# Optimization experiments

Measured on AMD Instinct MI355X. Metric: run time of the kernel, lower is better.

Reference implementation:

```python
import jax, jax.numpy as jnp
import numpy as np

B, S, K, D = 4096, 32, 1024, 128
DECAY, EPS = 0.99, 1e-05


def setup_inputs() -> dict:
    key = jax.random.key(0)
    k1, k2, k3 = jax.random.split(key, 3)
    indices = jax.random.randint(k1, (B, S), 0, K)
    embedding = jax.random.normal(k2, (S, K, D), dtype=jnp.float32)
    ema_cluster_size = jnp.zeros((S, K), dtype=jnp.float32)
    ema_w = jax.random.normal(k3, (S, K, D), dtype=jnp.float32)
    return {"indices": indices, "embedding": embedding,
            "ema_cluster_size": ema_cluster_size, "ema_w": ema_w}


def reference(indices, embedding, ema_cluster_size, ema_w):
    # embedding: [S, K, D]; indices: [B, S]
    s_idx = jnp.broadcast_to(jnp.arange(S), indices.shape)  # [B, S]

    # gather: z_q[b, s] = embedding[s, indices[b, s]]
    z_q = embedding[s_idx, indices]  # [B, S, D]

    # cluster_size = one_hot(indices, K).sum(0)  ==  histogram per state slot
    counts = jnp.zeros((S, K), embedding.dtype).at[s_idx, indices].add(1.0)

    # dw = einsum('bsk,bsd->skd', one_hot, z_q)  ==  scatter-add of z_q into codes
    dw = jnp.zeros((S, K, D), embedding.dtype).at[s_idx, indices].add(z_q)

    new_ecs = DECAY * ema_cluster_size + (1.0 - DECAY) * counts        # [S, K]
    new_ema_w = DECAY * ema_w + (1.0 - DECAY) * dw                     # [S, K, D]

    n = new_ecs.sum(axis=-1, keepdims=True)                            # [S, 1]
    cluster_size = (new_ecs + EPS) / (n + K * EPS) * n                 # Laplace-smoothed
    new_embedding = new_ema_w / cluster_size[..., None]                # [S, K, D]

    return z_q, new_embedding, new_ecs, new_ema_w
```

## Files before the change

### kernel.cpp

```cpp
#include <hip/hip_runtime.h>

#define B_ 4096
#define S_ 32
#define K_ 1024
#define D_ 128
constexpr float DECAY = 0.99f;
constexpr float OMD   = 0.01f;
constexpr float EPS   = 1e-5f;

typedef float f4 __attribute__((ext_vector_type(4)));
typedef int   i4 __attribute__((ext_vector_type(4)));


__global__ void __launch_bounds__(256)
init_kernel(const float* __restrict__ ecs_in,
            int* __restrict__ counts,
            float* __restrict__ n_out) {
    const int s = blockIdx.x;
    const int t = threadIdx.x;
    reinterpret_cast<i4*>(counts + s * K_)[t] = i4{0, 0, 0, 0};
    const f4 v = reinterpret_cast<const f4*>(ecs_in + s * K_)[t];
    float local = v.x + v.y + v.z + v.w;
#pragma unroll
    for (int off = 1; off < 64; off <<= 1) local += __shfl_xor(local, off);
    __shared__ float red[4];
    if ((t & 63) == 0) red[t >> 6] = local;
    __syncthreads();
    if (t == 0)
        n_out[s] = DECAY * (red[0] + red[1] + red[2] + red[3]) + OMD * (float)B_;
}

__global__ void __launch_bounds__(256)
gather_hist_kernel(const int* __restrict__ idx,
                   const float* __restrict__ emb,
                   float* __restrict__ z_q,
                   int* __restrict__ counts) {
    const int s     = blockIdx.x & (S_ - 1);
    const int chunk = blockIdx.x >> 5;
    const int g     = threadIdx.x >> 5;
    const int lane  = threadIdx.x & 31;
    const int b     = chunk * 8 + g;
    const int row   = b * S_ + s;
    const int k     = idx[row];
    if (lane == 0) atomicAdd(&counts[s * K_ + k], 1);
    const f4 val =
        reinterpret_cast<const f4*>(emb)[((size_t)s * K_ + k) * 32 + lane];
    __builtin_nontemporal_store(
        val, reinterpret_cast<f4*>(z_q) + (size_t)row * 32 + lane);
}

__global__ void __launch_bounds__(256)
ema_kernel(const float* __restrict__ ema_w,
           const float* __restrict__ emb,
           const float* __restrict__ ecs_in,
           const int* __restrict__ counts,
           const float* __restrict__ n_arr,
           float* __restrict__ new_ecs_out,
           float* __restrict__ new_ema_w_out,
           float* __restrict__ new_emb_out) {
    const int i = blockIdx.x;
    const int s = i & (S_ - 1);
    const int c = i >> 5;
    const size_t base = ((size_t)s * K_ + c * 32) * 32;
    const float n = n_arr[s];
    const float denom_inv = 1.0f / (n + (float)K_ * EPS);
#pragma unroll
    for (int it = 0; it < 4; ++it) {
        const size_t e = base + it * 256 + threadIdx.x;
        const int sk = (int)(e >> 5);
        const float ccount = (float)counts[sk];
        const float ne = DECAY * ecs_in[sk] + OMD * ccount;
        const float cs = (ne + EPS) * denom_inv * n;
        if ((e & 31) == 0) new_ecs_out[sk] = ne;

        const f4 w  = reinterpret_cast<const f4*>(ema_w)[e];
        const f4 em = reinterpret_cast<const f4*>(emb)[e];
        f4 nw;
        nw.x = DECAY * w.x + OMD * ccount * em.x;
        nw.y = DECAY * w.y + OMD * ccount * em.y;
        nw.z = DECAY * w.z + OMD * ccount * em.z;
        nw.w = DECAY * w.w + OMD * ccount * em.w;
        __builtin_nontemporal_store(
            nw, reinterpret_cast<f4*>(new_ema_w_out) + e);
        const float inv = 1.0f / cs;
        f4 nb;
        nb.x = nw.x * inv;
        nb.y = nw.y * inv;
        nb.z = nw.z * inv;
        nb.w = nw.w * inv;
        __builtin_nontemporal_store(
            nb, reinterpret_cast<f4*>(new_emb_out) + e);
    }
}

extern "C" void kernel_launch(void* const* d_in, const int* in_sizes, int n_in,
                              void* d_out, int out_size, void* d_ws, size_t ws_size,
                              hipStream_t stream) {
    const int*   idx   = (const int*)d_in[0];
    const float* emb   = (const float*)d_in[1];
    const float* ecs   = (const float*)d_in[2];
    const float* ema_w = (const float*)d_in[3];

    float* out       = (float*)d_out;
    float* z_q       = out;
    float* new_emb   = z_q + (size_t)B_ * S_ * D_;
    float* new_ecs   = new_emb + (size_t)S_ * K_ * D_;
    float* new_ema_w = new_ecs + (size_t)S_ * K_;

    int*   counts = (int*)d_ws;
    float* n_arr  = (float*)d_ws + (size_t)S_ * K_;

    init_kernel<<<S_, 256, 0, stream>>>(ecs, counts, n_arr);
    gather_hist_kernel<<<(B_ * S_) / 8, 256, 0, stream>>>(idx, emb, z_q, counts);
    ema_kernel<<<1024, 256, 0, stream>>>(
        ema_w, emb, ecs, counts, n_arr, new_ecs, new_ema_w, new_emb);
}
```

Before: 35.75 us.

## Replace global atomic histogram with transposed index buffer and per-block LDS histogram

The gather kernel now writes a transposed 16-bit copy of the indices per state slot instead of doing global atomics. The EMA kernel rebuilds each block's 32-code histogram in shared memory by scanning all B indices for its slot, and computes the per-slot sum inline, which removes the init kernel and one launch. In exchange, each EMA block redundantly reads 8 KB of indices and performs LDS atomics, and the gather grid is reduced to 2048 blocks.

```diff
diff --git a/kernel.cpp b/kernel.cpp
--- a/kernel.cpp
+++ b/kernel.cpp
@@ -8,8 +8,110 @@
 constexpr float OMD   = 0.01f;
 constexpr float EPS   = 1e-5f;
 
-typedef float f4 __attribute__((ext_vector_type(4)));
-typedef int   i4 __attribute__((ext_vector_type(4)));
+typedef float          f4  __attribute__((ext_vector_type(4)));
+typedef int            i4  __attribute__((ext_vector_type(4)));
+typedef unsigned short u16;
+typedef u16            us8 __attribute__((ext_vector_type(8)));
+
+
+__global__ void __launch_bounds__(256)
+gather_t_kernel(const int* __restrict__ idx,
+                const float* __restrict__ emb,
+                float* __restrict__ z_q,
+                u16* __restrict__ idx_t) {
+    const int s     = blockIdx.x & (S_ - 1);
+    const int chunk = blockIdx.x >> 5;
+    const int g     = threadIdx.x >> 5;
+    const int lane  = threadIdx.x & 31;
+    __shared__ int lds_k[64];
+#pragma unroll
+    for (int it = 0; it < 8; ++it) {
+        const int b   = chunk * 64 + it * 8 + g;
+        const int row = b * S_ + s;
+        const int k   = idx[row];
+        if (lane == 0) lds_k[it * 8 + g] = k;
+        const f4 val =
+            reinterpret_cast<const f4*>(emb)[((size_t)s * K_ + k) * 32 + lane];
+        __builtin_nontemporal_store(
+            val, reinterpret_cast<f4*>(z_q) + (size_t)row * 32 + lane);
+    }
+    __syncthreads();
+    if (threadIdx.x < 64)
+        idx_t[(size_t)s * B_ + chunk * 64 + threadIdx.x] =
+            (u16)lds_k[threadIdx.x];
+}
+
+__global__ void __launch_bounds__(256)
+ema_hist_kernel(const u16* __restrict__ idx_t,
+                const float* __restrict__ emb,
+                const float* __restrict__ ecs_in,
+                const float* __restrict__ ema_w,
+                float* __restrict__ new_ecs_out,
+                float* __restrict__ new_ema_w_out,
+                float* __restrict__ new_emb_out) {
+    const int s     = blockIdx.x & (S_ - 1);
+    const int c     = blockIdx.x >> 5;
+    const int t     = threadIdx.x;
+    const int kbase = c * 32;
+
+    __shared__ int   hist[32];
+    __shared__ float red[4];
+    __shared__ float n_sh;
+    if (t < 32) hist[t] = 0;
+    __syncthreads();
+
+    const us8* col = reinterpret_cast<const us8*>(idx_t + (size_t)s * B_);
+#pragma unroll
+    for (int it = 0; it < 2; ++it) {
+        const us8 v = col[it * 256 + t];
+#pragma unroll
+        for (int j = 0; j < 8; ++j) {
+            const unsigned u = (unsigned)v[j] - (unsigned)kbase;
+            if (u < 32u) atomicAdd(&hist[u], 1);
+        }
+    }
+
+    const f4 v = reinterpret_cast<const f4*>(ecs_in + s * K_)[t];
+    float local = v.x + v.y + v.z + v.w;
+#pragma unroll
+    for (int off = 1; off < 64; off <<= 1) local += __shfl_xor(local, off);
+    if ((t & 63) == 0) red[t >> 6] = local;
+    __syncthreads();
+    if (t == 0)
+        n_sh = DECAY * (red[0] + red[1] + red[2] + red[3]) + OMD * (float)B_;
+    __syncthreads();
+    const float n = n_sh;
+    const float denom_inv = 1.0f / (n + (float)K_ * EPS);
+
+    const size_t base = ((size_t)s * K_ + kbase) * 32;
+#pragma unroll
+    for (int it = 0; it < 4; ++it) {
+        const int    off = it * 256 + t;
+        const int    ub  = off >> 5;
+        const size_t e   = base + off;
+        const int    sk  = (int)(e >> 5);
+        const float ccount = (float)hist[ub];
+        const float ne = DECAY * ecs_in[sk] + OMD * ccount;
+        const float cs = (ne + EPS) * denom_inv * n;
+        if ((off & 31) == 0) new_ecs_out[sk] = ne;
+
+        const f4 w  = reinterpret_cast<const f4*>(ema_w)[e];
+        const f4 em = reinterpret_cast<const f4*>(emb)[e];
+        f4 nw;
+        nw.x = DECAY * w.x + OMD * ccount * em.x;
+        nw.y = DECAY * w.y + OMD * ccount * em.y;
+        nw.z = DECAY * w.z + OMD * ccount * em.z;
+        nw.w = DECAY * w.w + OMD * ccount * em.w;
+        __builtin_nontemporal_store(nw, reinterpret_cast<f4*>(new_ema_w_out) + e);
+        const float inv = 1.0f / cs;
+        f4 nb;
+        nb.x = nw.x * inv;
+        nb.y = nw.y * inv;
+        nb.z = nw.z * inv;
+        nb.w = nw.w * inv;
+        __builtin_nontemporal_store(nb, reinterpret_cast<f4*>(new_emb_out) + e);
+    }
+}
 
 
 __global__ void __launch_bounds__(256)
@@ -72,7 +174,6 @@
         const float ne = DECAY * ecs_in[sk] + OMD * ccount;
         const float cs = (ne + EPS) * denom_inv * n;
         if ((e & 31) == 0) new_ecs_out[sk] = ne;
-
         const f4 w  = reinterpret_cast<const f4*>(ema_w)[e];
         const f4 em = reinterpret_cast<const f4*>(emb)[e];
         f4 nw;
@@ -80,16 +181,14 @@
         nw.y = DECAY * w.y + OMD * ccount * em.y;
         nw.z = DECAY * w.z + OMD * ccount * em.z;
         nw.w = DECAY * w.w + OMD * ccount * em.w;
-        __builtin_nontemporal_store(
-            nw, reinterpret_cast<f4*>(new_ema_w_out) + e);
+        __builtin_nontemporal_store(nw, reinterpret_cast<f4*>(new_ema_w_out) + e);
         const float inv = 1.0f / cs;
         f4 nb;
         nb.x = nw.x * inv;
         nb.y = nw.y * inv;
         nb.z = nw.z * inv;
         nb.w = nw.w * inv;
-        __builtin_nontemporal_store(
-            nb, reinterpret_cast<f4*>(new_emb_out) + e);
+        __builtin_nontemporal_store(nb, reinterpret_cast<f4*>(new_emb_out) + e);
     }
 }
 
@@ -107,11 +206,17 @@
     float* new_ecs   = new_emb + (size_t)S_ * K_ * D_;
     float* new_ema_w = new_ecs + (size_t)S_ * K_;
 
-    int*   counts = (int*)d_ws;
-    float* n_arr  = (float*)d_ws + (size_t)S_ * K_;
-
-    init_kernel<<<S_, 256, 0, stream>>>(ecs, counts, n_arr);
-    gather_hist_kernel<<<(B_ * S_) / 8, 256, 0, stream>>>(idx, emb, z_q, counts);
-    ema_kernel<<<1024, 256, 0, stream>>>(
-        ema_w, emb, ecs, counts, n_arr, new_ecs, new_ema_w, new_emb);
-}
+    if (ws_size >= (size_t)B_ * S_ * sizeof(u16)) {
+        u16* idx_t = (u16*)d_ws;
+        gather_t_kernel<<<2048, 256, 0, stream>>>(idx, emb, z_q, idx_t);
+        ema_hist_kernel<<<1024, 256, 0, stream>>>(
+            idx_t, emb, ecs, ema_w, new_ecs, new_ema_w, new_emb);
+    } else {
+        int*   counts = (int*)d_ws;
+        float* n_arr  = (float*)d_ws + (size_t)S_ * K_;
+        init_kernel<<<S_, 256, 0, stream>>>(ecs, counts, n_arr);
+        gather_hist_kernel<<<(B_ * S_) / 8, 256, 0, stream>>>(idx, emb, z_q, counts);
+        ema_kernel<<<1024, 256, 0, stream>>>(
+            ema_w, emb, ecs, counts, n_arr, new_ecs, new_ema_w, new_emb);
+    }
+}
```

Result: faster. 31.52 us (-11.8%).

## Fuse three kernels into one with gather and local-histogram EMA block roles

Applied to the files above, without the earlier changes.

Replaces the init, gather-histogram, and EMA kernels with a single launch whose blocks take one of two roles. Gather blocks copy embedding rows into z_q, eight rows per warp group. EMA blocks each rebuild counts for their 16-code slice by scanning all B indices of their slot into a shared-memory histogram, then recompute n and write the EMA outputs. This removes two launch boundaries, the global counts buffer and its global atomics. In exchange, index reads are redundant: each EMA block reads 4096 indices, which adds about 8 MB of mostly cached traffic.

```diff
diff --git a/kernel.cpp b/kernel.cpp
--- a/kernel.cpp
+++ b/kernel.cpp
@@ -9,87 +9,101 @@
 constexpr float EPS   = 1e-5f;
 
 typedef float f4 __attribute__((ext_vector_type(4)));
-typedef int   i4 __attribute__((ext_vector_type(4)));
-
 
 __global__ void __launch_bounds__(256)
-init_kernel(const float* __restrict__ ecs_in,
-            int* __restrict__ counts,
-            float* __restrict__ n_out) {
-    const int s = blockIdx.x;
-    const int t = threadIdx.x;
-    reinterpret_cast<i4*>(counts + s * K_)[t] = i4{0, 0, 0, 0};
-    const f4 v = reinterpret_cast<const f4*>(ecs_in + s * K_)[t];
-    float local = v.x + v.y + v.z + v.w;
+fused_kernel(const int* __restrict__ idx,
+             const float* __restrict__ emb,
+             const float* __restrict__ ecs_in,
+             const float* __restrict__ ema_w,
+             float* __restrict__ z_q,
+             float* __restrict__ new_ecs_out,
+             float* __restrict__ new_ema_w_out,
+             float* __restrict__ new_emb_out) {
+    const int role = (blockIdx.x >> 3) & 1;
+    const int sub  = (int)(((blockIdx.x >> 4) << 3) | (blockIdx.x & 7));
+    const int t    = threadIdx.x;
+    const int s    = sub & (S_ - 1);
+
+    __shared__ int   hist[16];
+    __shared__ float red[4];
+    __shared__ float n_sh;
+
+    if (role == 0) {
+        const int chunk = sub >> 5;
+        const int g     = t >> 5;
+        const int lane  = t & 31;
+        int kk[8];
 #pragma unroll
-    for (int off = 1; off < 64; off <<= 1) local += __shfl_xor(local, off);
-    __shared__ float red[4];
-    if ((t & 63) == 0) red[t >> 6] = local;
-    __syncthreads();
-    if (t == 0)
-        n_out[s] = DECAY * (red[0] + red[1] + red[2] + red[3]) + OMD * (float)B_;
-}
+        for (int it = 0; it < 8; ++it) {
+            const int b = chunk * 64 + it * 8 + g;
+            kk[it] = idx[b * S_ + s];
+        }
+#pragma unroll
+        for (int it = 0; it < 8; ++it) {
+            const int b = chunk * 64 + it * 8 + g;
+            const f4 val =
+                reinterpret_cast<const f4*>(emb)[((size_t)s * K_ + kk[it]) * 32 + lane];
+            __builtin_nontemporal_store(
+                val, reinterpret_cast<f4*>(z_q) + ((size_t)b * S_ + s) * 32 + lane);
+        }
+    } else {
+        const int c     = sub >> 5;
+        const int kbase = c * 16;
+        if (t < 16) hist[t] = 0;
+        __syncthreads();
 
-__global__ void __launch_bounds__(256)
-gather_hist_kernel(const int* __restrict__ idx,
-                   const float* __restrict__ emb,
-                   float* __restrict__ z_q,
-                   int* __restrict__ counts) {
-    const int s     = blockIdx.x & (S_ - 1);
-    const int chunk = blockIdx.x >> 5;
-    const int g     = threadIdx.x >> 5;
-    const int lane  = threadIdx.x & 31;
-    const int b     = chunk * 8 + g;
-    const int row   = b * S_ + s;
-    const int k     = idx[row];
-    if (lane == 0) atomicAdd(&counts[s * K_ + k], 1);
-    const f4 val =
-        reinterpret_cast<const f4*>(emb)[((size_t)s * K_ + k) * 32 + lane];
-    __builtin_nontemporal_store(
-        val, reinterpret_cast<f4*>(z_q) + (size_t)row * 32 + lane);
-}
+        int kv[16];
+#pragma unroll
+        for (int j = 0; j < 16; ++j)
+            kv[j] = idx[(j * 256 + t) * S_ + s];
+#pragma unroll
+        for (int j = 0; j < 16; ++j) {
+            const unsigned u = (unsigned)kv[j] - (unsigned)kbase;
+            if (u < 16u) atomicAdd(&hist[u], 1);
+        }
 
-__global__ void __launch_bounds__(256)
-ema_kernel(const float* __restrict__ ema_w,
-           const float* __restrict__ emb,
-           const float* __restrict__ ecs_in,
-           const int* __restrict__ counts,
-           const float* __restrict__ n_arr,
-           float* __restrict__ new_ecs_out,
-           float* __restrict__ new_ema_w_out,
-           float* __restrict__ new_emb_out) {
-    const int i = blockIdx.x;
-    const int s = i & (S_ - 1);
-    const int c = i >> 5;
-    const size_t base = ((size_t)s * K_ + c * 32) * 32;
-    const float n = n_arr[s];
-    const float denom_inv = 1.0f / (n + (float)K_ * EPS);
+        const f4 v = reinterpret_cast<const f4*>(ecs_in + s * K_)[t];
+        float local = v.x + v.y + v.z + v.w;
 #pragma unroll
-    for (int it = 0; it < 4; ++it) {
-        const size_t e = base + it * 256 + threadIdx.x;
-        const int sk = (int)(e >> 5);
-        const float ccount = (float)counts[sk];
-        const float ne = DECAY * ecs_in[sk] + OMD * ccount;
-        const float cs = (ne + EPS) * denom_inv * n;
-        if ((e & 31) == 0) new_ecs_out[sk] = ne;
+        for (int off = 1; off < 64; off <<= 1) local += __shfl_xor(local, off);
+        if ((t & 63) == 0) red[t >> 6] = local;
+        __syncthreads();
+        if (t == 0)
+            n_sh = DECAY * (red[0] + red[1] + red[2] + red[3]) + OMD * (float)B_;
+        __syncthreads();
+        const float n = n_sh;
+        const float denom_inv = 1.0f / (n + (float)K_ * EPS);
 
-        const f4 w  = reinterpret_cast<const f4*>(ema_w)[e];
-        const f4 em = reinterpret_cast<const f4*>(emb)[e];
-        f4 nw;
-        nw.x = DECAY * w.x + OMD * ccount * em.x;
-        nw.y = DECAY * w.y + OMD * ccount * em.y;
-        nw.z = DECAY * w.z + OMD * ccount * em.z;
-        nw.w = DECAY * w.w + OMD * ccount * em.w;
-        __builtin_nontemporal_store(
-            nw, reinterpret_cast<f4*>(new_ema_w_out) + e);
-        const float inv = 1.0f / cs;
-        f4 nb;
-        nb.x = nw.x * inv;
-        nb.y = nw.y * inv;
-        nb.z = nw.z * inv;
-        nb.w = nw.w * inv;
-        __builtin_nontemporal_store(
-            nb, reinterpret_cast<f4*>(new_emb_out) + e);
+        const size_t base = ((size_t)s * K_ + kbase) * 32;
+#pragma unroll
+        for (int it = 0; it < 2; ++it) {
+            const int    off = it * 256 + t;
+            const int    ub  = off >> 5;
+            const size_t e   = base + off;
+            const int    sk  = (int)(e >> 5);
+            const float ccount = (float)hist[ub];
+            const float ne = DECAY * ecs_in[sk] + OMD * ccount;
+            const float cs = (ne + EPS) * denom_inv * n;
+            if ((off & 31) == 0) new_ecs_out[sk] = ne;
+
+            const f4 w  = reinterpret_cast<const f4*>(ema_w)[e];
+            const f4 em = reinterpret_cast<const f4*>(emb)[e];
+            f4 nw;
+            nw.x = DECAY * w.x + OMD * ccount * em.x;
+            nw.y = DECAY * w.y + OMD * ccount * em.y;
+            nw.z = DECAY * w.z + OMD * ccount * em.z;
+            nw.w = DECAY * w.w + OMD * ccount * em.w;
+            __builtin_nontemporal_store(
+                nw, reinterpret_cast<f4*>(new_ema_w_out) + e);
+            const float inv = 1.0f / cs;
+            f4 nb;
+            nb.x = nw.x * inv;
+            nb.y = nw.y * inv;
+            nb.z = nw.z * inv;
+            nb.w = nw.w * inv;
+            __builtin_nontemporal_store(
+                nb, reinterpret_cast<f4*>(new_emb_out) + e);
+        }
     }
 }
 
@@ -107,11 +121,6 @@
     float* new_ecs   = new_emb + (size_t)S_ * K_ * D_;
     float* new_ema_w = new_ecs + (size_t)S_ * K_;
 
-    int*   counts = (int*)d_ws;
-    float* n_arr  = (float*)d_ws + (size_t)S_ * K_;
-
-    init_kernel<<<S_, 256, 0, stream>>>(ecs, counts, n_arr);
-    gather_hist_kernel<<<(B_ * S_) / 8, 256, 0, stream>>>(idx, emb, z_q, counts);
-    ema_kernel<<<1024, 256, 0, stream>>>(
-        ema_w, emb, ecs, counts, n_arr, new_ecs, new_ema_w, new_emb);
+    fused_kernel<<<4096, 256, 0, stream>>>(
+        idx, emb, ecs, ema_w, z_q, new_ecs, new_ema_w, new_emb);
 }
```

Result: slower. 58.87 us (+64.7%).
